# Kernel tuning notes

Hardware: AMD Instinct MI355X
Metric: run time of the kernel (lower is better)

## Reference

```python
import jax, jax.numpy as jnp
import numpy as np

B, S, D, H = 4, 2048, 1024, 16
DK = D // H

def setup_inputs() -> dict:
    key = jax.random.key(0)
    ks = jax.random.split(key, 9)
    s = 1.0 / np.sqrt(D)
    return {
        "x":  jax.random.normal(ks[0], (B, S, D), dtype=jnp.float32),
        "Wq": jax.random.uniform(ks[1], (D, D), jnp.float32, -s, s),
        "bq": jax.random.uniform(ks[2], (D,), jnp.float32, -s, s),
        "Wk": jax.random.uniform(ks[3], (D, D), jnp.float32, -s, s),
        "bk": jax.random.uniform(ks[4], (D,), jnp.float32, -s, s),
        "Wv": jax.random.uniform(ks[5], (D, D), jnp.float32, -s, s),
        "bv": jax.random.uniform(ks[6], (D,), jnp.float32, -s, s),
        "Wo": jax.random.uniform(ks[7], (D, D), jnp.float32, -s, s),
        "bo": jax.random.uniform(ks[8], (D,), jnp.float32, -s, s),
    }

def reference(x, Wq, bq, Wk, bk, Wv, bv, Wo, bo):
    # Q/K/V projections: [B,S,D] -> [B,H,S,DK]
    def proj(W, b):
        return (x @ W.T + b).reshape(B, S, H, DK).transpose(0, 2, 1, 3)
    Q, K, V = proj(Wq, bq), proj(Wk, bk), proj(Wv, bv)
    scale = 1.0 / np.sqrt(DK).astype(np.float32)
    scores = jnp.einsum('bhqd,bhkd->bhqk', Q, K) * scale  # [B,H,S,S]
    attn = jax.nn.softmax(scores, axis=-1)                 # dropout = identity (eval)
    out = jnp.einsum('bhqk,bhkd->bhqd', attn, V)           # [B,H,S,DK]
    out = out.transpose(0, 2, 1, 3).reshape(B, S, D)
    return out @ Wo.T + bo, attn
```

## Files before the change

### kernel.cpp

```cpp
#include <hip/hip_runtime.h>
#include <hip/hip_bf16.h>

#define Bb 4
#define Ss 2048
#define Dd 1024
#define Hh 16
#define DKk 64

typedef float f32x4 __attribute__((ext_vector_type(4)));
typedef short bf16x8 __attribute__((ext_vector_type(8)));
typedef unsigned short u16x4 __attribute__((ext_vector_type(4)));

#define MFMA16(a, b, c) __builtin_amdgcn_mfma_f32_16x16x32_bf16((a), (b), (c), 0, 0, 0)

__device__ __forceinline__ unsigned short f2bf(float f) {
  union { float f; unsigned u; } v;
  v.f = f;
  unsigned r = v.u + 0x7FFFu + ((v.u >> 16) & 1u);
  return (unsigned short)(r >> 16);
}

__device__ __forceinline__ float bf2f(unsigned short h) {
  union { unsigned u; float f; } v;
  v.u = ((unsigned)h) << 16;
  return v.f;
}

__device__ __forceinline__ float fast_exp2(float x) {
  float r;
  asm("v_exp_f32 %0, %1" : "=v"(r) : "v"(x));
  return r;
}

__device__ __forceinline__ bf16x8 cvt8(float4 f0, float4 f1) {
  bf16x8 r;
  r[0] = (short)f2bf(f0.x); r[1] = (short)f2bf(f0.y);
  r[2] = (short)f2bf(f0.z); r[3] = (short)f2bf(f0.w);
  r[4] = (short)f2bf(f1.x); r[5] = (short)f2bf(f1.y);
  r[6] = (short)f2bf(f1.z); r[7] = (short)f2bf(f1.w);
  return r;
}

__global__ __launch_bounds__(256) void cast_all(
    const float* __restrict__ x,  const float* __restrict__ Wq,
    const float* __restrict__ Wk, const float* __restrict__ Wv,
    const float* __restrict__ Wo,
    unsigned short* __restrict__ xb,  unsigned short* __restrict__ wqb,
    unsigned short* __restrict__ wkb, unsigned short* __restrict__ wvb,
    unsigned short* __restrict__ wob)
{
  int bid = blockIdx.x;
  const float* s; unsigned short* d; size_t base8;
  if (bid < 4096) { s = x; d = xb; base8 = (size_t)bid * 256; }
  else {
    int t = bid - 4096; int w = t >> 9; int off = t & 511;
    s = (w == 0) ? Wq : (w == 1) ? Wk : (w == 2) ? Wv : Wo;
    d = (w == 0) ? wqb : (w == 1) ? wkb : (w == 2) ? wvb : wob;
    base8 = (size_t)off * 256;
  }
  size_t i8 = base8 + threadIdx.x;
  const float4* sp = (const float4*)s + 2 * i8;
  float4 a = sp[0], b = sp[1];
  *(bf16x8*)(d + i8 * 8) = cvt8(a, b);
}

__global__ __launch_bounds__(256) void qkv_kernel(
    const unsigned short* __restrict__ xb,
    const unsigned short* __restrict__ wqb, const float* __restrict__ bq,
    const unsigned short* __restrict__ wkb, const float* __restrict__ bk_,
    const unsigned short* __restrict__ wvb, const float* __restrict__ bv_,
    unsigned short* __restrict__ qo, unsigned short* __restrict__ ko,
    unsigned short* __restrict__ vto)
{
  __shared__ __align__(16) unsigned short Al[128 * 64];
  __shared__ __align__(16) unsigned short Bl[128 * 64];
  const int tid = threadIdx.x, lane = tid & 63, wid = tid >> 6;
  const int m0 = blockIdx.x * 128;
  const int sel = blockIdx.y >> 3;
  const int n0 = (blockIdx.y & 7) * 128;
  const unsigned short* W; const float* bias;
  if (sel == 0)      { W = wqb; bias = bq;  }
  else if (sel == 1) { W = wkb; bias = bk_; }
  else               { W = wvb; bias = bv_; }
  const float prescale = (sel == 0) ? 0.125f : 1.0f;

  const int wm = (wid >> 1) * 64, wn = (wid & 1) * 64;
  const int lr = lane & 15, lk8 = (lane >> 4) * 8;

  f32x4 acc[4][4] = {};
  const unsigned short* Abase = xb + (size_t)m0 * Dd;
  const unsigned short* Bbase = W + (size_t)n0 * Dd;

  for (int k0 = 0; k0 < Dd; k0 += 64) {
#pragma unroll
    for (int i = 0; i < 4; ++i) {
      int qq = (wid * 4 + i) * 64 + lane;
      int row = qq >> 3, c8 = qq & 7;
      const unsigned short* ga = Abase + (size_t)row * Dd + k0 + c8 * 8;
      const unsigned short* gb = Bbase + (size_t)row * Dd + k0 + c8 * 8;
      __builtin_amdgcn_global_load_lds(
          (const __attribute__((address_space(1))) unsigned int*)ga,
          (__attribute__((address_space(3))) unsigned int*)(Al + (wid * 4 + i) * 512),
          16, 0, 0);
      __builtin_amdgcn_global_load_lds(
          (const __attribute__((address_space(1))) unsigned int*)gb,
          (__attribute__((address_space(3))) unsigned int*)(Bl + (wid * 4 + i) * 512),
          16, 0, 0);
    }
    __syncthreads();
#pragma unroll
    for (int ks = 0; ks < 2; ++ks) {
      bf16x8 av[4], bv[4];
#pragma unroll
      for (int i = 0; i < 4; ++i)
        av[i] = *(const bf16x8*)&Al[(wm + i * 16 + lr) * 64 + ks * 32 + lk8];
#pragma unroll
      for (int j = 0; j < 4; ++j)
        bv[j] = *(const bf16x8*)&Bl[(wn + j * 16 + lr) * 64 + ks * 32 + lk8];
#pragma unroll
      for (int i = 0; i < 4; ++i)
#pragma unroll
        for (int j = 0; j < 4; ++j)
          acc[i][j] = MFMA16(av[i], bv[j], acc[i][j]);
    }
    __syncthreads();
  }

  const int rg = (lane >> 4) * 4;
  if (sel < 2) {
    unsigned short* out = (sel == 0) ? qo : ko;
#pragma unroll
    for (int i = 0; i < 4; ++i)
#pragma unroll
      for (int j = 0; j < 4; ++j) {
        int n = n0 + wn + j * 16 + lr;
        float bvv = bias[n];
        int hh = n >> 6, dk = n & 63;
#pragma unroll
        for (int r = 0; r < 4; ++r) {
          int m = m0 + wm + i * 16 + rg + r;
          int bb = m >> 11, ss = m & (Ss - 1);
          float v = (acc[i][j][r] + bvv) * prescale;
          out[((size_t)(bb * Hh + hh) * Ss + ss) * DKk + dk] = f2bf(v);
        }
      }
  } else {
#pragma unroll
    for (int i = 0; i < 4; ++i) {
      int m_base = m0 + wm + i * 16 + rg;
      int bb = m_base >> 11, ss0 = m_base & (Ss - 1);
#pragma unroll
      for (int j = 0; j < 4; ++j) {
        int n = n0 + wn + j * 16 + lr;
        float bvv = bias[n];
        int hh = n >> 6, dk = n & 63;
        u16x4 pk;
#pragma unroll
        for (int r = 0; r < 4; ++r) pk[r] = f2bf(acc[i][j][r] + bvv);
        *(u16x4*)&vto[((size_t)(bb * Hh + hh) * DKk + dk) * Ss + ss0] = pk;
      }
    }
  }
}

__global__ __launch_bounds__(256) void attn_kernel(
    const unsigned short* __restrict__ Qw, const unsigned short* __restrict__ Kw,
    const unsigned short* __restrict__ Vt, float* __restrict__ attn,
    unsigned short* __restrict__ OH)
{
  __shared__ unsigned short Pl[4][32][72];
  const int tid = threadIdx.x, lane = tid & 63, wid = tid >> 6;
  const int L = blockIdx.x;
  const int bh = (L & 7) + 8 * (L >> 7);
  const int qb = (L >> 3) & 15;
  const int q0 = qb * 128 + wid * 32;
  const unsigned short* Qh = Qw + (size_t)bh * Ss * DKk;
  const unsigned short* Kh = Kw + (size_t)bh * Ss * DKk;
  const unsigned short* Vh = Vt + (size_t)bh * DKk * Ss;
  const int lr = lane & 15;
  const int lk8 = (lane >> 4) * 8;
  const int rg = (lane >> 4) * 4;
  const float L2E = 1.44269504088896f;

  bf16x8 aq[2][2];
#pragma unroll
  for (int mi = 0; mi < 2; ++mi)
#pragma unroll
    for (int ks = 0; ks < 2; ++ks)
      aq[mi][ks] = *(const bf16x8*)&Qh[(size_t)(q0 + mi * 16 + lr) * DKk + ks * 32 + lk8];

  float lsum[2] = {0.f, 0.f};
  for (int kb = 0; kb < Ss; kb += 64) {
    bf16x8 bk[4][2];
#pragma unroll
    for (int nj = 0; nj < 4; ++nj)
#pragma unroll
      for (int ks = 0; ks < 2; ++ks)
        bk[nj][ks] = *(const bf16x8*)&Kh[(size_t)(kb + nj * 16 + lr) * DKk + ks * 32 + lk8];
#pragma unroll
    for (int mi = 0; mi < 2; ++mi) {
      float acc = 0.f;
#pragma unroll
      for (int nj = 0; nj < 4; ++nj) {
        f32x4 c = {};
        c = MFMA16(bk[nj][0], aq[mi][0], c);
        c = MFMA16(bk[nj][1], aq[mi][1], c);
        acc += fast_exp2(c[0] * L2E) + fast_exp2(c[1] * L2E) +
               fast_exp2(c[2] * L2E) + fast_exp2(c[3] * L2E);
      }
      lsum[mi] += acc;
    }
  }
  float linv[2];
#pragma unroll
  for (int mi = 0; mi < 2; ++mi) {
    float l = lsum[mi];
    l += __shfl_xor(l, 16, 64);
    l += __shfl_xor(l, 32, 64);
    linv[mi] = 1.0f / l;
  }

  f32x4 o[2][4] = {};
  float* attn_bh = attn + (size_t)bh * Ss * Ss;
  for (int kb = 0; kb < Ss; kb += 64) {
    bf16x8 bk[4][2], bvv[4][2];
#pragma unroll
    for (int nj = 0; nj < 4; ++nj)
#pragma unroll
      for (int ks = 0; ks < 2; ++ks) {
        bk[nj][ks] = *(const bf16x8*)&Kh[(size_t)(kb + nj * 16 + lr) * DKk + ks * 32 + lk8];
        bvv[nj][ks] = *(const bf16x8*)&Vh[(size_t)(nj * 16 + lr) * Ss + kb + ks * 32 + lk8];
      }

#pragma unroll
    for (int mi = 0; mi < 2; ++mi) {
      const float li = linv[mi];
#pragma unroll
      for (int nj = 0; nj < 4; ++nj) {
        f32x4 c = {};
        c = MFMA16(bk[nj][0], aq[mi][0], c);
        c = MFMA16(bk[nj][1], aq[mi][1], c);
        float p0 = fast_exp2(c[0] * L2E) * li;
        float p1 = fast_exp2(c[1] * L2E) * li;
        float p2 = fast_exp2(c[2] * L2E) * li;
        float p3 = fast_exp2(c[3] * L2E) * li;
        unsigned w0 = (unsigned)f2bf(p0) | ((unsigned)f2bf(p1) << 16);
        unsigned w1 = (unsigned)f2bf(p2) | ((unsigned)f2bf(p3) << 16);
        uint2 w = {w0, w1};
        *(uint2*)&Pl[wid][mi * 16 + lr][nj * 16 + rg] = w;
      }
    }
#pragma unroll
    for (int ks = 0; ks < 2; ++ks) {
      const int kk = ks * 32 + lk8;
      bf16x8 ap[2];
#pragma unroll
      for (int mi = 0; mi < 2; ++mi)
        ap[mi] = *(const bf16x8*)&Pl[wid][mi * 16 + lr][kk];
#pragma unroll
      for (int mi = 0; mi < 2; ++mi)
#pragma unroll
        for (int nj = 0; nj < 4; ++nj)
          o[mi][nj] = MFMA16(ap[mi], bvv[nj][ks], o[mi][nj]);
    }
    {
      const int c4 = (lane & 15) * 4;
      const int rsub = lane >> 4;
#pragma unroll
      for (int i = 0; i < 8; ++i) {
        int row = i * 4 + rsub;
        u16x4 pb4 = *(const u16x4*)&Pl[wid][row][c4];
        f32x4 pf;
        pf[0] = bf2f(pb4[0]); pf[1] = bf2f(pb4[1]);
        pf[2] = bf2f(pb4[2]); pf[3] = bf2f(pb4[3]);
        __builtin_nontemporal_store(pf,
            (f32x4*)(attn_bh + (size_t)(q0 + row) * Ss + kb + c4));
      }
    }
  }

  const int b = bh >> 4, h = bh & 15;
#pragma unroll
  for (int mi = 0; mi < 2; ++mi)
#pragma unroll
    for (int nj = 0; nj < 4; ++nj)
#pragma unroll
      for (int r = 0; r < 4; ++r) {
        int q = q0 + mi * 16 + rg + r;
        int d = nj * 16 + lr;
        OH[(((size_t)b * Ss + q) * Hh + h) * DKk + d] = f2bf(o[mi][nj][r]);
      }
}

__global__ __launch_bounds__(256) void oproj_kernel(
    const unsigned short* __restrict__ A, const unsigned short* __restrict__ W,
    const float* __restrict__ bias, float* __restrict__ out)
{
  __shared__ __align__(16) unsigned short Al[128 * 64];
  __shared__ __align__(16) unsigned short Bl[128 * 64];
  const int tid = threadIdx.x, lane = tid & 63, wid = tid >> 6;
  const int m0 = blockIdx.x * 128;
  const int n0 = blockIdx.y * 128;
  const int wm = (wid >> 1) * 64, wn = (wid & 1) * 64;
  const int lr = lane & 15, lk8 = (lane >> 4) * 8;

  f32x4 acc[4][4] = {};
  const unsigned short* Abase = A + (size_t)m0 * Dd;
  const unsigned short* Bbase = W + (size_t)n0 * Dd;

  for (int k0 = 0; k0 < Dd; k0 += 64) {
#pragma unroll
    for (int i = 0; i < 4; ++i) {
      int qq = (wid * 4 + i) * 64 + lane;
      int row = qq >> 3, c8 = qq & 7;
      const unsigned short* ga = Abase + (size_t)row * Dd + k0 + c8 * 8;
      const unsigned short* gb = Bbase + (size_t)row * Dd + k0 + c8 * 8;
      __builtin_amdgcn_global_load_lds(
          (const __attribute__((address_space(1))) unsigned int*)ga,
          (__attribute__((address_space(3))) unsigned int*)(Al + (wid * 4 + i) * 512),
          16, 0, 0);
      __builtin_amdgcn_global_load_lds(
          (const __attribute__((address_space(1))) unsigned int*)gb,
          (__attribute__((address_space(3))) unsigned int*)(Bl + (wid * 4 + i) * 512),
          16, 0, 0);
    }
    __syncthreads();
#pragma unroll
    for (int ks = 0; ks < 2; ++ks) {
      bf16x8 av[4], bv[4];
#pragma unroll
      for (int i = 0; i < 4; ++i)
        av[i] = *(const bf16x8*)&Al[(wm + i * 16 + lr) * 64 + ks * 32 + lk8];
#pragma unroll
      for (int j = 0; j < 4; ++j)
        bv[j] = *(const bf16x8*)&Bl[(wn + j * 16 + lr) * 64 + ks * 32 + lk8];
#pragma unroll
      for (int i = 0; i < 4; ++i)
#pragma unroll
        for (int j = 0; j < 4; ++j)
          acc[i][j] = MFMA16(av[i], bv[j], acc[i][j]);
    }
    __syncthreads();
  }

  const int rg = (lane >> 4) * 4;
#pragma unroll
  for (int i = 0; i < 4; ++i)
#pragma unroll
    for (int j = 0; j < 4; ++j) {
      int n = n0 + wn + j * 16 + lr;
      float bvv = bias[n];
#pragma unroll
      for (int r = 0; r < 4; ++r) {
        int m = m0 + wm + i * 16 + rg + r;
        out[(size_t)m * Dd + n] = acc[i][j][r] + bvv;
      }
    }
}

extern "C" void kernel_launch(void* const* d_in, const int* in_sizes, int n_in,
                              void* d_out, int out_size, void* d_ws, size_t ws_size,
                              hipStream_t stream) {
  const float* x  = (const float*)d_in[0];
  const float* Wq = (const float*)d_in[1];
  const float* bq = (const float*)d_in[2];
  const float* Wk = (const float*)d_in[3];
  const float* bk = (const float*)d_in[4];
  const float* Wv = (const float*)d_in[5];
  const float* bv = (const float*)d_in[6];
  const float* Wo = (const float*)d_in[7];
  const float* bo = (const float*)d_in[8];

  float* out  = (float*)d_out;
  float* attn = out + (size_t)Bb * Ss * Dd;

  const size_t headElems = (size_t)Bb * Hh * Ss * DKk;
  const size_t wElems = (size_t)Dd * Dd;
  unsigned short* qws  = (unsigned short*)d_ws;
  unsigned short* kws  = qws + headElems;
  unsigned short* vtws = kws + headElems;
  unsigned short* ohw  = vtws + headElems;
  unsigned short* xb   = ohw + headElems;
  unsigned short* wqb  = xb + headElems;
  unsigned short* wkb  = wqb + wElems;
  unsigned short* wvb  = wkb + wElems;
  unsigned short* wob  = wvb + wElems;

  dim3 blk(256);
  cast_all<<<dim3(6144), blk, 0, stream>>>(x, Wq, Wk, Wv, Wo, xb, wqb, wkb, wvb, wob);
  qkv_kernel<<<dim3(64, 24), blk, 0, stream>>>(xb, wqb, bq, wkb, bk, wvb, bv,
                                               qws, kws, vtws);
  attn_kernel<<<dim3(1024), blk, 0, stream>>>(qws, kws, vtws, attn, ohw);
  oproj_kernel<<<dim3(64, 8), blk, 0, stream>>>(ohw, wob, bo, out);
}
```

Measured before the change: 500.2 us.

## Double-buffer K loads in attention and fold log2e into Q prescale

K fragments are now prefetched one 64-key tile ahead using two register buffers, so global loads overlap the MFMA and exp work in both the row-sum pass and the output pass. The log2(e) factor is folded into the Q projection prescale, which removes a multiply before every exp2. The bf16 packing of probabilities uses the hardware v_cvt_pk_bf16_f32 instruction, and the attn store is moved ahead of the P·V MFMAs. The extra buffers raise register pressure, which may lower occupancy.

```diff
diff --git a/kernel.cpp b/kernel.cpp
--- a/kernel.cpp
+++ b/kernel.cpp
@@ -29,6 +29,12 @@
 __device__ __forceinline__ float fast_exp2(float x) {
   float r;
   asm("v_exp_f32 %0, %1" : "=v"(r) : "v"(x));
+  return r;
+}
+
+__device__ __forceinline__ unsigned cvt_pk_bf16(float lo, float hi) {
+  unsigned r;
+  asm("v_cvt_pk_bf16_f32 %0, %1, %2" : "=v"(r) : "v"(lo), "v"(hi));
   return r;
 }
 
@@ -82,7 +88,7 @@
   if (sel == 0)      { W = wqb; bias = bq;  }
   else if (sel == 1) { W = wkb; bias = bk_; }
   else               { W = wvb; bias = bv_; }
-  const float prescale = (sel == 0) ? 0.125f : 1.0f;
+  const float prescale = (sel == 0) ? 0.180336880111f : 1.0f;
 
   const int wm = (wid >> 1) * 64, wn = (wid & 1) * 64;
   const int lr = lane & 15, lk8 = (lane >> 4) * 8;
@@ -180,7 +186,6 @@
   const int lr = lane & 15;
   const int lk8 = (lane >> 4) * 8;
   const int rg = (lane >> 4) * 4;
-  const float L2E = 1.44269504088896f;
 
   bf16x8 aq[2][2];
 #pragma unroll
@@ -189,26 +194,41 @@
     for (int ks = 0; ks < 2; ++ks)
       aq[mi][ks] = *(const bf16x8*)&Qh[(size_t)(q0 + mi * 16 + lr) * DKk + ks * 32 + lk8];
 
+#define LOADK(dst, kbase)                                                       \
+  {                                                                             \
+    _Pragma("unroll")                                                           \
+    for (int nj = 0; nj < 4; ++nj) {                                            \
+      _Pragma("unroll")                                                         \
+      for (int ks = 0; ks < 2; ++ks)                                            \
+        dst[nj][ks] = *(const bf16x8*)&Kh[(size_t)((kbase) + nj * 16 + lr) * DKk \
+                                          + ks * 32 + lk8];                     \
+    }                                                                           \
+  }
+
   float lsum[2] = {0.f, 0.f};
-  for (int kb = 0; kb < Ss; kb += 64) {
-    bf16x8 bk[4][2];
-#pragma unroll
-    for (int nj = 0; nj < 4; ++nj)
-#pragma unroll
-      for (int ks = 0; ks < 2; ++ks)
-        bk[nj][ks] = *(const bf16x8*)&Kh[(size_t)(kb + nj * 16 + lr) * DKk + ks * 32 + lk8];
-#pragma unroll
-    for (int mi = 0; mi < 2; ++mi) {
-      float acc = 0.f;
-#pragma unroll
-      for (int nj = 0; nj < 4; ++nj) {
-        f32x4 c = {};
-        c = MFMA16(bk[nj][0], aq[mi][0], c);
-        c = MFMA16(bk[nj][1], aq[mi][1], c);
-        acc += fast_exp2(c[0] * L2E) + fast_exp2(c[1] * L2E) +
-               fast_exp2(c[2] * L2E) + fast_exp2(c[3] * L2E);
-      }
-      lsum[mi] += acc;
+  {
+    bf16x8 kA[4][2], kB[4][2];
+    LOADK(kA, 0);
+    auto body1 = [&](bf16x8 (&bkt)[4][2], int kb) {
+#pragma unroll
+      for (int mi = 0; mi < 2; ++mi) {
+        float acc = 0.f;
+#pragma unroll
+        for (int nj = 0; nj < 4; ++nj) {
+          f32x4 c = {};
+          c = MFMA16(bkt[nj][0], aq[mi][0], c);
+          c = MFMA16(bkt[nj][1], aq[mi][1], c);
+          acc += fast_exp2(c[0]) + fast_exp2(c[1]) +
+                 fast_exp2(c[2]) + fast_exp2(c[3]);
+        }
+        lsum[mi] += acc;
+      }
+    };
+    for (int kb = 0; kb < Ss; kb += 128) {
+      LOADK(kB, kb + 64);
+      body1(kA, kb);
+      if (kb + 128 < Ss) LOADK(kA, kb + 128);
+      body1(kB, kb + 64);
     }
   }
   float linv[2];
@@ -222,50 +242,35 @@
 
   f32x4 o[2][4] = {};
   float* attn_bh = attn + (size_t)bh * Ss * Ss;
-  for (int kb = 0; kb < Ss; kb += 64) {
-    bf16x8 bk[4][2], bvv[4][2];
-#pragma unroll
-    for (int nj = 0; nj < 4; ++nj)
-#pragma unroll
-      for (int ks = 0; ks < 2; ++ks) {
-        bk[nj][ks] = *(const bf16x8*)&Kh[(size_t)(kb + nj * 16 + lr) * DKk + ks * 32 + lk8];
-        bvv[nj][ks] = *(const bf16x8*)&Vh[(size_t)(nj * 16 + lr) * Ss + kb + ks * 32 + lk8];
-      }
-
-#pragma unroll
-    for (int mi = 0; mi < 2; ++mi) {
-      const float li = linv[mi];
-#pragma unroll
-      for (int nj = 0; nj < 4; ++nj) {
-        f32x4 c = {};
-        c = MFMA16(bk[nj][0], aq[mi][0], c);
-        c = MFMA16(bk[nj][1], aq[mi][1], c);
-        float p0 = fast_exp2(c[0] * L2E) * li;
-        float p1 = fast_exp2(c[1] * L2E) * li;
-        float p2 = fast_exp2(c[2] * L2E) * li;
-        float p3 = fast_exp2(c[3] * L2E) * li;
-        unsigned w0 = (unsigned)f2bf(p0) | ((unsigned)f2bf(p1) << 16);
-        unsigned w1 = (unsigned)f2bf(p2) | ((unsigned)f2bf(p3) << 16);
-        uint2 w = {w0, w1};
-        *(uint2*)&Pl[wid][mi * 16 + lr][nj * 16 + rg] = w;
-      }
-    }
-#pragma unroll
-    for (int ks = 0; ks < 2; ++ks) {
-      const int kk = ks * 32 + lk8;
-      bf16x8 ap[2];
-#pragma unroll
-      for (int mi = 0; mi < 2; ++mi)
-        ap[mi] = *(const bf16x8*)&Pl[wid][mi * 16 + lr][kk];
-#pragma unroll
-      for (int mi = 0; mi < 2; ++mi)
-#pragma unroll
-        for (int nj = 0; nj < 4; ++nj)
-          o[mi][nj] = MFMA16(ap[mi], bvv[nj][ks], o[mi][nj]);
-    }
-    {
-      const int c4 = (lane & 15) * 4;
-      const int rsub = lane >> 4;
+  {
+    bf16x8 kA[4][2], kB[4][2];
+    LOADK(kA, 0);
+    const int c4 = (lane & 15) * 4;
+    const int rsub = lane >> 4;
+    auto body2 = [&](bf16x8 (&bkt)[4][2], int kb) {
+      bf16x8 bvv[4][2];
+#pragma unroll
+      for (int nj = 0; nj < 4; ++nj)
+#pragma unroll
+        for (int ks = 0; ks < 2; ++ks)
+          bvv[nj][ks] = *(const bf16x8*)&Vh[(size_t)(nj * 16 + lr) * Ss + kb + ks * 32 + lk8];
+
+#pragma unroll
+      for (int mi = 0; mi < 2; ++mi) {
+        const float li = linv[mi];
+#pragma unroll
+        for (int nj = 0; nj < 4; ++nj) {
+          f32x4 c = {};
+          c = MFMA16(bkt[nj][0], aq[mi][0], c);
+          c = MFMA16(bkt[nj][1], aq[mi][1], c);
+          float p0 = fast_exp2(c[0]) * li;
+          float p1 = fast_exp2(c[1]) * li;
+          float p2 = fast_exp2(c[2]) * li;
+          float p3 = fast_exp2(c[3]) * li;
+          uint2 w = {cvt_pk_bf16(p0, p1), cvt_pk_bf16(p2, p3)};
+          *(uint2*)&Pl[wid][mi * 16 + lr][nj * 16 + rg] = w;
+        }
+      }
 #pragma unroll
       for (int i = 0; i < 8; ++i) {
         int row = i * 4 + rsub;
@@ -276,8 +281,28 @@
         __builtin_nontemporal_store(pf,
             (f32x4*)(attn_bh + (size_t)(q0 + row) * Ss + kb + c4));
       }
-    }
-  }
+#pragma unroll
+      for (int ks = 0; ks < 2; ++ks) {
+        const int kk = ks * 32 + lk8;
+        bf16x8 ap[2];
+#pragma unroll
+        for (int mi = 0; mi < 2; ++mi)
+          ap[mi] = *(const bf16x8*)&Pl[wid][mi * 16 + lr][kk];
+#pragma unroll
+        for (int mi = 0; mi < 2; ++mi)
+#pragma unroll
+          for (int nj = 0; nj < 4; ++nj)
+            o[mi][nj] = MFMA16(ap[mi], bvv[nj][ks], o[mi][nj]);
+      }
+    };
+    for (int kb = 0; kb < Ss; kb += 128) {
+      LOADK(kB, kb + 64);
+      body2(kA, kb);
+      if (kb + 128 < Ss) LOADK(kA, kb + 128);
+      body2(kB, kb + 64);
+    }
+  }
+#undef LOADK
 
   const int b = bh >> 4, h = bh & 15;
 #pragma unroll
```

After: 502.8 us. Within noise of the previous version (+0.5%).
